# Kernel tuning notes

Measured on AMD Instinct MI355X. Metric: run time of the kernel, lower is better.

The kernel has to match this reference:

```python
import jax, jax.numpy as jnp
import numpy as np

EMBED_DIM = 1024
NUM_HEADS = 16
HEAD_DIM = EMBED_DIM // NUM_HEADS


def setup_inputs() -> dict:
    key = jax.random.key(0)
    k1, k2, k3 = jax.random.split(key, 3)
    scale = 1.0 / np.sqrt(EMBED_DIM)
    x = jax.random.normal(k1, (2, 2048, EMBED_DIM), dtype=jnp.float32)
    w_qkv = jax.random.normal(k2, (EMBED_DIM, 3 * EMBED_DIM), dtype=jnp.float32) * scale
    b_qkv = jnp.zeros((3 * EMBED_DIM,), dtype=jnp.float32)
    w_out = jax.random.normal(k3, (EMBED_DIM, EMBED_DIM), dtype=jnp.float32) * scale
    b_out = jnp.zeros((EMBED_DIM,), dtype=jnp.float32)
    return {"x": x, "w_qkv": w_qkv, "b_qkv": b_qkv, "w_out": w_out, "b_out": b_out}


def reference(x, w_qkv, b_qkv, w_out, b_out):
    B, N, C = x.shape
    H, D = NUM_HEADS, HEAD_DIM
    qkv = x @ w_qkv + b_qkv                      # [B, N, 3C]
    qkv = qkv.reshape(B, N, 3, H, D)
    q = qkv[:, :, 0].transpose(0, 2, 1, 3)       # [B, H, N, D]
    k = qkv[:, :, 1].transpose(0, 2, 1, 3)
    v = qkv[:, :, 2].transpose(0, 2, 1, 3)
    scores = jnp.einsum('bhnd,bhmd->bhnm', q, k) / jnp.sqrt(jnp.float32(D))
    attn = jax.nn.softmax(scores, axis=-1)
    out = jnp.einsum('bhnm,bhmd->bhnd', attn, v)  # [B, H, N, D]
    out = out.transpose(0, 2, 1, 3).reshape(B, N, C)
    return out @ w_out + b_out
```

## Files before the change

### kernel.cpp

```cpp
#include <hip/hip_runtime.h>
#include <stdint.h>

typedef unsigned short u16;
typedef short s16x8 __attribute__((ext_vector_type(8)));
typedef unsigned short u16x8 __attribute__((ext_vector_type(8)));
typedef unsigned short u16x4 __attribute__((ext_vector_type(4)));
typedef float f32x4 __attribute__((ext_vector_type(4)));
typedef float f32x16 __attribute__((ext_vector_type(16)));
typedef unsigned int u32x2 __attribute__((ext_vector_type(2)));
typedef unsigned int u32x4 __attribute__((ext_vector_type(4)));

#if __has_builtin(__builtin_amdgcn_exp2f)
#define EXP2F(x) __builtin_amdgcn_exp2f(x)
#else
#define EXP2F(x) exp2f(x)
#endif

#define QSCALE 0.18033688011112042f

__device__ __forceinline__ u16 f2b(float f) {
  union { float f; uint32_t u; } v; v.f = f;
  uint32_t r = (v.u + 0x7fffu + ((v.u >> 16) & 1u)) >> 16;
  return (u16)r;
}

__device__ __forceinline__ uint32_t pkhi(uint32_t hi, uint32_t lo) {
#if __has_builtin(__builtin_amdgcn_perm)
  return __builtin_amdgcn_perm(hi, lo, 0x07060302u);
#else
  return (lo >> 16) | (hi & 0xffff0000u);
#endif
}

__device__ __forceinline__ void plswap(uint32_t& a, uint32_t& b) {
#if __has_builtin(__builtin_amdgcn_permlane32_swap)
  typedef unsigned int uv2 __attribute__((ext_vector_type(2)));
  uv2 r = __builtin_amdgcn_permlane32_swap(a, b, false, false);
  a = r[0];
  b = r[1];
#else
  asm volatile("v_permlane32_swap_b32 %0, %1" : "+v"(a), "+v"(b));
#endif
}

__device__ __forceinline__ void sync_lds() {
  asm volatile("s_waitcnt lgkmcnt(0)\ns_barrier" ::: "memory");
}

__device__ __forceinline__ void gld16(const void* g, void* l) {
  __builtin_amdgcn_global_load_lds((__attribute__((address_space(1))) void*)g,
                                   (__attribute__((address_space(3))) void*)l,
                                   16, 0, 0);
}

__global__ __launch_bounds__(256)
void prep(const float* __restrict__ x, u16* __restrict__ xb,
          const float* __restrict__ w_qkv, u16* __restrict__ wqT,
          const float* __restrict__ w_out, u16* __restrict__ woT) {
  __shared__ float tile[32][33];
  const int bid = blockIdx.x;
  const int t = threadIdx.x;
  if (bid < 2048) {
    const size_t i = ((size_t)bid * 256 + t) * 8;
    f32x4 v0 = *(const f32x4*)(x + i);
    f32x4 v1 = *(const f32x4*)(x + i + 4);
    u16x8 u;
#pragma unroll
    for (int j = 0; j < 4; j++) { u[j] = f2b(v0[j]); u[4 + j] = f2b(v1[j]); }
    *(u16x8*)(xb + i) = u;
    return;
  }
  const float* src;
  u16* dst;
  int N, nb, kb;
  if (bid < 5120) {
    const int b2 = bid - 2048;
    src = w_qkv; dst = wqT; N = 3072;
    nb = (b2 % 96) * 32; kb = (b2 / 96) * 32;
  } else {
    const int b3 = bid - 5120;
    src = w_out; dst = woT; N = 1024;
    nb = (b3 & 31) * 32; kb = (b3 >> 5) * 32;
  }
  const int tx = t & 31, ty = t >> 5;
#pragma unroll
  for (int i = 0; i < 4; i++)
    tile[ty + i * 8][tx] = src[(size_t)(kb + ty + i * 8) * N + nb + tx];
  __syncthreads();
#pragma unroll
  for (int i = 0; i < 4; i++)
    dst[(size_t)(nb + ty + i * 8) * 1024 + kb + tx] = f2b(tile[tx][ty + i * 8]);
}

template <int EPI, int WN>
__global__ __launch_bounds__(256, 3)
void gemm_bt(const u16* __restrict__ A, const u16* __restrict__ Bt,
             const float* __restrict__ bias, float* __restrict__ outF,
             u16* __restrict__ outQ, u16* __restrict__ outK,
             u16* __restrict__ outVt, int M, int N, int K) {
  constexpr int BN = WN * 64;
  constexpr int RW = 4 / WN;
  constexpr int MI = 128 / RW / 16;
  constexpr int NBI = WN * 2;
  constexpr int SMEM = (EPI == 0) ? 34816 : (16384 + WN * 8192);
  __shared__ char smem[SMEM];
  u16* As = (u16*)smem;
  u16* Bs = As + 128 * 64;

  const int t = threadIdx.x;
  const int m0 = blockIdx.y * 128, n0 = blockIdx.x * BN;
  const int w = t >> 6, lane = t & 63;
  const int wm = w / WN, wn = w % WN;
  const int quad = lane >> 4, lrow = lane & 15;
  const int r8 = lane >> 3, s8 = lane & 7;
  const int csw = (s8 ^ r8) * 8;

  const u16* gA = A + (size_t)(m0 + w * 32 + r8) * K + csw;
  const u16* gB = Bt + (size_t)(n0 + w * (WN * 16) + r8) * K + csw;
  u16* wAs = As + (w * 32 + r8) * 64 + s8 * 8;
  u16* wBs = Bs + (w * (WN * 16) + r8) * 64 + s8 * 8;

  f32x4 acc[MI][4];
#pragma unroll
  for (int i = 0; i < MI; i++)
#pragma unroll
    for (int j = 0; j < 4; j++) {
      f32x4 z = {0.f, 0.f, 0.f, 0.f};
      acc[i][j] = z;
    }

  u16x8 pa[4], pb[NBI];
#pragma unroll
  for (int i = 0; i < 4; i++) pa[i] = *(const u16x8*)(gA + (size_t)(i * 8) * K);
#pragma unroll
  for (int i = 0; i < NBI; i++) pb[i] = *(const u16x8*)(gB + (size_t)(i * 8) * K);

  const int KT = K >> 6;
  for (int kt = 0; kt < KT; ++kt) {
    sync_lds();
#pragma unroll
    for (int i = 0; i < 4; i++) *(u16x8*)(wAs + i * 8 * 64) = pa[i];
#pragma unroll
    for (int i = 0; i < NBI; i++) *(u16x8*)(wBs + i * 8 * 64) = pb[i];
    if (kt + 1 < KT) {
      const size_t off = (size_t)(kt + 1) * 64;
#pragma unroll
      for (int i = 0; i < 4; i++)
        pa[i] = *(const u16x8*)(gA + (size_t)(i * 8) * K + off);
#pragma unroll
      for (int i = 0; i < NBI; i++)
        pb[i] = *(const u16x8*)(gB + (size_t)(i * 8) * K + off);
    }
    sync_lds();

#pragma unroll
    for (int ks = 0; ks < 2; ks++) {
      s16x8 a[MI], b[4];
#pragma unroll
      for (int i = 0; i < MI; i++)
        a[i] = *(const s16x8*)&As[(wm * (MI * 16) + i * 16 + lrow) * 64 +
                                  (((ks * 4 + quad) ^ (lrow & 7)) * 8)];
#pragma unroll
      for (int j = 0; j < 4; j++)
        b[j] = *(const s16x8*)&Bs[(wn * 64 + j * 16 + lrow) * 64 +
                                  (((ks * 4 + quad) ^ (lrow & 7)) * 8)];
#pragma unroll
      for (int i = 0; i < MI; i++)
#pragma unroll
        for (int j = 0; j < 4; j++)
          acc[i][j] = __builtin_amdgcn_mfma_f32_16x16x32_bf16(a[i], b[j],
                                                              acc[i][j], 0, 0, 0);
    }
  }

  if (EPI == 1) {
#pragma unroll
    for (int i = 0; i < MI; i++) {
      const int row = m0 + wm * (MI * 16) + i * 16 + quad * 4;
#pragma unroll
      for (int j = 0; j < 4; j++) {
        const int col = n0 + wn * 64 + j * 16 + lrow;
        const float bv = bias[col];
#pragma unroll
        for (int r = 0; r < 4; r++)
          outF[(size_t)(row + r) * N + col] = acc[i][j][r] + bv;
      }
    }
    return;
  }

  sync_lds();
  u16* rp = (u16*)smem + w * (64 * 68);
  const int cb = n0 + wn * 64;
  const int which = cb >> 10;
  const int h = (cb & 1023) >> 6;
  const int rbase = m0 + wm * 64;
  const int bb = rbase >> 11, nn0 = rbase & 2047;
  const int rl = lane >> 3, cc = (lane & 7) * 8;

  if (which != 2) {
    const float s = (which == 0) ? QSCALE : 1.0f;
#pragma unroll
    for (int i = 0; i < 4; i++)
#pragma unroll
      for (int j = 0; j < 4; j++) {
        const float bv = bias[cb + j * 16 + lrow];
#pragma unroll
        for (int r = 0; r < 4; r++)
          rp[(i * 16 + quad * 4 + r) * 68 + j * 16 + lrow] =
              f2b((acc[i][j][r] + bv) * s);
      }
    u16* dst = ((which == 0) ? outQ : outK) +
               ((size_t)(bb * 16 + h) * 2048 + nn0) * 64;
#pragma unroll
    for (int it = 0; it < 8; it++) {
      const int row = it * 8 + rl;
      *(u16x8*)&dst[(size_t)row * 64 + cc] = *(const u16x8*)&rp[row * 68 + cc];
    }
  } else {
#pragma unroll
    for (int i = 0; i < 4; i++)
#pragma unroll
      for (int j = 0; j < 4; j++) {
        const float bv = bias[cb + j * 16 + lrow];
        u16x4 pk;
#pragma unroll
        for (int r = 0; r < 4; r++) pk[r] = f2b(acc[i][j][r] + bv);
        *(u16x4*)&rp[(j * 16 + lrow) * 68 + i * 16 + quad * 4] = pk;
      }
    u16* dst = outVt + ((size_t)(bb * 16 + h) * 64) * 2048 + nn0;
#pragma unroll
    for (int it = 0; it < 8; it++) {
      const int d = it * 8 + rl;
      *(u16x8*)&dst[(size_t)d * 2048 + cc] = *(const u16x8*)&rp[d * 68 + cc];
    }
  }
}

__global__ __launch_bounds__(256)
void attn_kernel(const u16* __restrict__ Q, const u16* __restrict__ Kg,
                 const u16* __restrict__ Vt, u16* __restrict__ AO) {
  __shared__ u16 Ks[2][64 * 64];
  __shared__ u16 Vs[2][64 * 64];

  const int t = threadIdx.x;
  const int bh = blockIdx.x;
  const int qt = blockIdx.y;
  const int w = t >> 6, lane = t & 63;
  const int l31 = lane & 31, lh = lane >> 5;
  const int srow8 = lane >> 3, chunk = lane & 7;
  const int csw = chunk ^ srow8;
  const size_t base = (size_t)bh * 2048 * 64;

  s16x8 qf[4];
  {
    const u16* qp = Q + base + (size_t)(qt * 128 + w * 32 + l31) * 64 + lh * 8;
#pragma unroll
    for (int ks = 0; ks < 4; ks++) qf[ks] = *(const s16x8*)(qp + ks * 16);
  }

  int cx[4];
#pragma unroll
  for (int ks = 0; ks < 4; ks++) cx[ks] = ((2 * ks + lh) ^ (l31 & 7)) * 8;

  const u16* kgl = Kg + base + (size_t)(w * 16 + srow8) * 64 + csw * 8;
  const u16* vgl = Vt + base + (size_t)(w * 16 + srow8) * 2048 + csw * 8;
  const int lbase = (w * 16) * 64;

  const short one_bf16 = 0x3F80;
  s16x8 ones = {one_bf16, one_bf16, one_bf16, one_bf16,
                one_bf16, one_bf16, one_bf16, one_bf16};

  f32x16 ot0, ot1, liacc;
#pragma unroll
  for (int e = 0; e < 16; e++) { ot0[e] = 0.f; ot1[e] = 0.f; liacc[e] = 0.f; }

  gld16(kgl, &Ks[0][lbase]);
  gld16(kgl + 512, &Ks[0][lbase + 512]);
  gld16(vgl, &Vs[0][lbase]);
  gld16(vgl + (size_t)8 * 2048, &Vs[0][lbase + 512]);

  for (int kt = 0; kt < 32; kt++) {
    const int cur = kt & 1;
    __syncthreads();
    if (kt + 1 < 32) {
      const int nxt = cur ^ 1;
      gld16(kgl + (size_t)(kt + 1) * 4096, &Ks[nxt][lbase]);
      gld16(kgl + (size_t)(kt + 1) * 4096 + 512, &Ks[nxt][lbase + 512]);
      gld16(vgl + (kt + 1) * 64, &Vs[nxt][lbase]);
      gld16(vgl + (kt + 1) * 64 + (size_t)8 * 2048, &Vs[nxt][lbase + 512]);
    }

    f32x16 sc0, sc1;
#pragma unroll
    for (int e = 0; e < 16; e++) { sc0[e] = 0.f; sc1[e] = 0.f; }
#pragma unroll
    for (int ks = 0; ks < 4; ks++) {
      s16x8 k0 = *(const s16x8*)&Ks[cur][l31 * 64 + cx[ks]];
      s16x8 k1 = *(const s16x8*)&Ks[cur][(32 + l31) * 64 + cx[ks]];
      sc0 = __builtin_amdgcn_mfma_f32_32x32x16_bf16(k0, qf[ks], sc0, 0, 0, 0);
      sc1 = __builtin_amdgcn_mfma_f32_32x32x16_bf16(k1, qf[ks], sc1, 0, 0, 0);
    }

    uint32_t P[2][4][2];
#pragma unroll
    for (int tb = 0; tb < 2; tb++) {
      const f32x16& s = tb ? sc1 : sc0;
#pragma unroll
      for (int g = 0; g < 4; g++) {
        uint32_t u[4];
#pragma unroll
        for (int r = 0; r < 4; r++)
          u[r] = __builtin_bit_cast(uint32_t, EXP2F(s[g * 4 + r]));
        P[tb][g][0] = pkhi(u[1], u[0]);
        P[tb][g][1] = pkhi(u[3], u[2]);
      }
    }

#pragma unroll
    for (int tb = 0; tb < 2; tb++) {
#pragma unroll
      for (int gp = 0; gp < 2; gp++) {
        uint32_t w0 = P[tb][2 * gp][0], w2 = P[tb][2 * gp + 1][0];
        uint32_t w1 = P[tb][2 * gp][1], w3 = P[tb][2 * gp + 1][1];
        plswap(w0, w2);
        plswap(w1, w3);
        u32x4 fw = {w0, w1, w2, w3};
        s16x8 pf = __builtin_bit_cast(s16x8, fw);
        const int ks = tb * 2 + gp;
        s16x8 v0 = *(const s16x8*)&Vs[cur][l31 * 64 + cx[ks]];
        s16x8 v1 = *(const s16x8*)&Vs[cur][(32 + l31) * 64 + cx[ks]];
        ot0 = __builtin_amdgcn_mfma_f32_32x32x16_bf16(v0, pf, ot0, 0, 0, 0);
        ot1 = __builtin_amdgcn_mfma_f32_32x32x16_bf16(v1, pf, ot1, 0, 0, 0);
        liacc = __builtin_amdgcn_mfma_f32_32x32x16_bf16(ones, pf, liacc, 0, 0, 0);
      }
    }
  }

  const float inv = 1.0f / liacc[0];
  const int bb = bh >> 4, h = bh & 15;
  const int qn = qt * 128 + w * 32 + l31;
  u16* dst = AO + (size_t)(bb * 2048 + qn) * 1024 + h * 64;
#pragma unroll
  for (int db = 0; db < 2; db++) {
    const f32x16& o = db ? ot1 : ot0;
#pragma unroll
    for (int g = 0; g < 4; g++) {
      u16x4 pk;
#pragma unroll
      for (int r = 0; r < 4; r++) pk[r] = f2b(o[g * 4 + r] * inv);
      *(u16x4*)&dst[db * 32 + g * 8 + lh * 4] = pk;
    }
  }
}

extern "C" void kernel_launch(void* const* d_in, const int* in_sizes, int n_in,
                              void* d_out, int out_size, void* d_ws,
                              size_t ws_size, hipStream_t stream) {
  const float* x     = (const float*)d_in[0];
  const float* w_qkv = (const float*)d_in[1];
  const float* b_qkv = (const float*)d_in[2];
  const float* w_out = (const float*)d_in[3];
  const float* b_out = (const float*)d_in[4];
  float* out = (float*)d_out;

  char* ws = (char*)d_ws;
  u16* wqT = (u16*)ws; ws += (size_t)3072 * 1024 * 2;
  u16* woT = (u16*)ws; ws += (size_t)1024 * 1024 * 2;
  u16* q   = (u16*)ws; ws += (size_t)32 * 2048 * 64 * 2;
  u16* k   = (u16*)ws; ws += (size_t)32 * 2048 * 64 * 2;
  u16* vt  = (u16*)ws; ws += (size_t)32 * 64 * 2048 * 2;
  u16* xb  = (u16*)ws; ws += (size_t)4096 * 1024 * 2;
  u16* ao  = xb;

  prep<<<dim3(6144), 256, 0, stream>>>(x, xb, w_qkv, wqT, w_out, woT);
  gemm_bt<0, 2><<<dim3(24, 32), 256, 0, stream>>>(xb, wqT, b_qkv, nullptr, q, k,
                                                  vt, 4096, 3072, 1024);
  attn_kernel<<<dim3(32, 16), 256, 0, stream>>>(q, k, vt, ao);
  gemm_bt<1, 1><<<dim3(16, 32), 256, 0, stream>>>(ao, woT, b_out, out, nullptr,
                                                  nullptr, nullptr, 4096, 1024, 1024);
}
```

Measured before the change: 182.7 us.

## Split attention keys across two waves with register-direct K/V loads

Rewrites the attention kernel so each 128-thread block handles 64 queries. The two waves each process half of the key sequence, loading K and V fragments straight from global memory into registers, where the old kernel used double-buffered LDS staging with block barriers. The row sum is now accumulated in scalar registers rather than through an extra MFMA against a ones vector. Partial outputs are merged through shared memory at the end. This removes per-tile barriers and LDS traffic, at the cost of uncoalesced global loads with no LDS reuse, doubled K/V reads across query tiles, and a final reduction.

After: 192.0 us. 1.05x slower.

```diff
diff --git a/kernel.cpp b/kernel.cpp
--- a/kernel.cpp
+++ b/kernel.cpp
@@ -45,12 +45,6 @@
 
 __device__ __forceinline__ void sync_lds() {
   asm volatile("s_waitcnt lgkmcnt(0)\ns_barrier" ::: "memory");
-}
-
-__device__ __forceinline__ void gld16(const void* g, void* l) {
-  __builtin_amdgcn_global_load_lds((__attribute__((address_space(1))) void*)g,
-                                   (__attribute__((address_space(3))) void*)l,
-                                   16, 0, 0);
 }
 
 __global__ __launch_bounds__(256)
@@ -237,119 +231,150 @@
   }
 }
 
-__global__ __launch_bounds__(256)
+__global__ __launch_bounds__(128, 2)
 void attn_kernel(const u16* __restrict__ Q, const u16* __restrict__ Kg,
                  const u16* __restrict__ Vt, u16* __restrict__ AO) {
-  __shared__ u16 Ks[2][64 * 64];
-  __shared__ u16 Vs[2][64 * 64];
+  __shared__ float Osh[64][64];
+  __shared__ float Lsh[2][32];
 
   const int t = threadIdx.x;
   const int bh = blockIdx.x;
   const int qt = blockIdx.y;
   const int w = t >> 6, lane = t & 63;
   const int l31 = lane & 31, lh = lane >> 5;
-  const int srow8 = lane >> 3, chunk = lane & 7;
-  const int csw = chunk ^ srow8;
   const size_t base = (size_t)bh * 2048 * 64;
 
-  s16x8 qf[4];
-  {
-    const u16* qp = Q + base + (size_t)(qt * 128 + w * 32 + l31) * 64 + lh * 8;
-#pragma unroll
-    for (int ks = 0; ks < 4; ks++) qf[ks] = *(const s16x8*)(qp + ks * 16);
-  }
-
-  int cx[4];
-#pragma unroll
-  for (int ks = 0; ks < 4; ks++) cx[ks] = ((2 * ks + lh) ^ (l31 & 7)) * 8;
-
-  const u16* kgl = Kg + base + (size_t)(w * 16 + srow8) * 64 + csw * 8;
-  const u16* vgl = Vt + base + (size_t)(w * 16 + srow8) * 2048 + csw * 8;
-  const int lbase = (w * 16) * 64;
-
-  const short one_bf16 = 0x3F80;
-  s16x8 ones = {one_bf16, one_bf16, one_bf16, one_bf16,
-                one_bf16, one_bf16, one_bf16, one_bf16};
-
-  f32x16 ot0, ot1, liacc;
-#pragma unroll
-  for (int e = 0; e < 16; e++) { ot0[e] = 0.f; ot1[e] = 0.f; liacc[e] = 0.f; }
-
-  gld16(kgl, &Ks[0][lbase]);
-  gld16(kgl + 512, &Ks[0][lbase + 512]);
-  gld16(vgl, &Vs[0][lbase]);
-  gld16(vgl + (size_t)8 * 2048, &Vs[0][lbase + 512]);
+  s16x8 qf[2][4];
+#pragma unroll
+  for (int qg = 0; qg < 2; qg++) {
+    const u16* qp =
+        Q + base + (size_t)(qt * 64 + qg * 32 + l31) * 64 + lh * 8;
+#pragma unroll
+    for (int ks = 0; ks < 4; ks++) qf[qg][ks] = *(const s16x8*)(qp + ks * 16);
+  }
+
+  const u16* kp = Kg + base + (size_t)(w * 1024 + l31) * 64 + lh * 8;
+  const u16* vp = Vt + base + (size_t)l31 * 2048 + w * 1024 + lh * 8;
+
+  f32x16 ot[2][2];
+#pragma unroll
+  for (int qg = 0; qg < 2; qg++)
+#pragma unroll
+    for (int dt = 0; dt < 2; dt++)
+#pragma unroll
+      for (int e = 0; e < 16; e++) ot[qg][dt][e] = 0.f;
+  float li[2] = {0.f, 0.f};
+
+  s16x8 kf[4], vf[2][2];
+#pragma unroll
+  for (int ks = 0; ks < 4; ks++) kf[ks] = *(const s16x8*)(kp + ks * 16);
+#pragma unroll
+  for (int dt = 0; dt < 2; dt++)
+#pragma unroll
+    for (int s = 0; s < 2; s++)
+      vf[dt][s] = *(const s16x8*)(vp + (size_t)dt * 32 * 2048 + s * 16);
 
   for (int kt = 0; kt < 32; kt++) {
-    const int cur = kt & 1;
-    __syncthreads();
+    f32x16 sc[2];
+#pragma unroll
+    for (int qg = 0; qg < 2; qg++)
+#pragma unroll
+      for (int e = 0; e < 16; e++) sc[qg][e] = 0.f;
+#pragma unroll
+    for (int ks = 0; ks < 4; ks++) {
+      sc[0] = __builtin_amdgcn_mfma_f32_32x32x16_bf16(kf[ks], qf[0][ks], sc[0], 0, 0, 0);
+      sc[1] = __builtin_amdgcn_mfma_f32_32x32x16_bf16(kf[ks], qf[1][ks], sc[1], 0, 0, 0);
+    }
     if (kt + 1 < 32) {
-      const int nxt = cur ^ 1;
-      gld16(kgl + (size_t)(kt + 1) * 4096, &Ks[nxt][lbase]);
-      gld16(kgl + (size_t)(kt + 1) * 4096 + 512, &Ks[nxt][lbase + 512]);
-      gld16(vgl + (kt + 1) * 64, &Vs[nxt][lbase]);
-      gld16(vgl + (kt + 1) * 64 + (size_t)8 * 2048, &Vs[nxt][lbase + 512]);
-    }
-
-    f32x16 sc0, sc1;
-#pragma unroll
-    for (int e = 0; e < 16; e++) { sc0[e] = 0.f; sc1[e] = 0.f; }
-#pragma unroll
-    for (int ks = 0; ks < 4; ks++) {
-      s16x8 k0 = *(const s16x8*)&Ks[cur][l31 * 64 + cx[ks]];
-      s16x8 k1 = *(const s16x8*)&Ks[cur][(32 + l31) * 64 + cx[ks]];
-      sc0 = __builtin_amdgcn_mfma_f32_32x32x16_bf16(k0, qf[ks], sc0, 0, 0, 0);
-      sc1 = __builtin_amdgcn_mfma_f32_32x32x16_bf16(k1, qf[ks], sc1, 0, 0, 0);
+      const u16* kn = kp + (size_t)(kt + 1) * 2048;
+#pragma unroll
+      for (int ks = 0; ks < 4; ks++) kf[ks] = *(const s16x8*)(kn + ks * 16);
     }
 
     uint32_t P[2][4][2];
 #pragma unroll
-    for (int tb = 0; tb < 2; tb++) {
-      const f32x16& s = tb ? sc1 : sc0;
+    for (int qg = 0; qg < 2; qg++) {
+      float rsum = 0.f;
 #pragma unroll
       for (int g = 0; g < 4; g++) {
         uint32_t u[4];
 #pragma unroll
-        for (int r = 0; r < 4; r++)
-          u[r] = __builtin_bit_cast(uint32_t, EXP2F(s[g * 4 + r]));
-        P[tb][g][0] = pkhi(u[1], u[0]);
-        P[tb][g][1] = pkhi(u[3], u[2]);
-      }
-    }
-
-#pragma unroll
-    for (int tb = 0; tb < 2; tb++) {
-#pragma unroll
-      for (int gp = 0; gp < 2; gp++) {
-        uint32_t w0 = P[tb][2 * gp][0], w2 = P[tb][2 * gp + 1][0];
-        uint32_t w1 = P[tb][2 * gp][1], w3 = P[tb][2 * gp + 1][1];
+        for (int r = 0; r < 4; r++) {
+          u[r] = __builtin_bit_cast(uint32_t, EXP2F(sc[qg][g * 4 + r]));
+          rsum += __builtin_bit_cast(float, u[r] & 0xffff0000u);
+        }
+        P[qg][g][0] = pkhi(u[1], u[0]);
+        P[qg][g][1] = pkhi(u[3], u[2]);
+      }
+      li[qg] += rsum;
+    }
+
+#pragma unroll
+    for (int gp = 0; gp < 2; gp++) {
+      s16x8 pf[2];
+#pragma unroll
+      for (int qg = 0; qg < 2; qg++) {
+        uint32_t w0 = P[qg][2 * gp][0], w2 = P[qg][2 * gp + 1][0];
+        uint32_t w1 = P[qg][2 * gp][1], w3 = P[qg][2 * gp + 1][1];
         plswap(w0, w2);
         plswap(w1, w3);
         u32x4 fw = {w0, w1, w2, w3};
-        s16x8 pf = __builtin_bit_cast(s16x8, fw);
-        const int ks = tb * 2 + gp;
-        s16x8 v0 = *(const s16x8*)&Vs[cur][l31 * 64 + cx[ks]];
-        s16x8 v1 = *(const s16x8*)&Vs[cur][(32 + l31) * 64 + cx[ks]];
-        ot0 = __builtin_amdgcn_mfma_f32_32x32x16_bf16(v0, pf, ot0, 0, 0, 0);
-        ot1 = __builtin_amdgcn_mfma_f32_32x32x16_bf16(v1, pf, ot1, 0, 0, 0);
-        liacc = __builtin_amdgcn_mfma_f32_32x32x16_bf16(ones, pf, liacc, 0, 0, 0);
-      }
-    }
-  }
-
-  const float inv = 1.0f / liacc[0];
-  const int bb = bh >> 4, h = bh & 15;
-  const int qn = qt * 128 + w * 32 + l31;
-  u16* dst = AO + (size_t)(bb * 2048 + qn) * 1024 + h * 64;
-#pragma unroll
-  for (int db = 0; db < 2; db++) {
-    const f32x16& o = db ? ot1 : ot0;
-#pragma unroll
-    for (int g = 0; g < 4; g++) {
-      u16x4 pk;
-#pragma unroll
-      for (int r = 0; r < 4; r++) pk[r] = f2b(o[g * 4 + r] * inv);
-      *(u16x4*)&dst[db * 32 + g * 8 + lh * 4] = pk;
+        pf[qg] = __builtin_bit_cast(s16x8, fw);
+      }
+#pragma unroll
+      for (int dt = 0; dt < 2; dt++) {
+        ot[0][dt] = __builtin_amdgcn_mfma_f32_32x32x16_bf16(vf[dt][gp], pf[0], ot[0][dt], 0, 0, 0);
+        ot[1][dt] = __builtin_amdgcn_mfma_f32_32x32x16_bf16(vf[dt][gp], pf[1], ot[1][dt], 0, 0, 0);
+      }
+    }
+    if (kt + 1 < 32) {
+      const u16* vn = vp + (kt + 1) * 32;
+#pragma unroll
+      for (int dt = 0; dt < 2; dt++)
+#pragma unroll
+        for (int s = 0; s < 2; s++)
+          vf[dt][s] = *(const s16x8*)(vn + (size_t)dt * 32 * 2048 + s * 16);
+    }
+  }
+
+  float lifull[2];
+#pragma unroll
+  for (int qg = 0; qg < 2; qg++)
+    lifull[qg] = li[qg] + __shfl_xor(li[qg], 32);
+
+  if (w == 1) {
+#pragma unroll
+    for (int qg = 0; qg < 2; qg++) {
+#pragma unroll
+      for (int dt = 0; dt < 2; dt++)
+#pragma unroll
+        for (int e = 0; e < 16; e++)
+          Osh[qg * 32 + dt * 16 + e][lane] = ot[qg][dt][e];
+      if (lh == 0) Lsh[qg][l31] = lifull[qg];
+    }
+  }
+  __syncthreads();
+  if (w == 0) {
+    const int bb = bh >> 4, h = bh & 15;
+#pragma unroll
+    for (int qg = 0; qg < 2; qg++) {
+      const float inv = 1.0f / (lifull[qg] + Lsh[qg][l31]);
+      const int qn = qt * 64 + qg * 32 + l31;
+      u16* dst = AO + (size_t)(bb * 2048 + qn) * 1024 + h * 64;
+#pragma unroll
+      for (int dt = 0; dt < 2; dt++) {
+#pragma unroll
+        for (int g = 0; g < 4; g++) {
+          u16x4 pk;
+#pragma unroll
+          for (int r = 0; r < 4; r++) {
+            const float v =
+                ot[qg][dt][g * 4 + r] + Osh[qg * 32 + dt * 16 + g * 4 + r][lane];
+            pk[r] = f2b(v * inv);
+          }
+          *(u16x4*)&dst[dt * 32 + g * 8 + lh * 4] = pk;
+        }
+      }
     }
   }
 }
@@ -376,7 +401,7 @@
   prep<<<dim3(6144), 256, 0, stream>>>(x, xb, w_qkv, wqT, w_out, woT);
   gemm_bt<0, 2><<<dim3(24, 32), 256, 0, stream>>>(xb, wqT, b_qkv, nullptr, q, k,
                                                   vt, 4096, 3072, 1024);
-  attn_kernel<<<dim3(32, 16), 256, 0, stream>>>(q, k, vt, ao);
+  attn_kernel<<<dim3(32, 32), 128, 0, stream>>>(q, k, vt, ao);
   gemm_bt<1, 1><<<dim3(16, 32), 256, 0, stream>>>(ao, woT, b_out, out, nullptr,
                                                   nullptr, nullptr, 4096, 1024, 1024);
 }
```

## Split attention KV sequence across two wave groups per block and merge

Applied to the files above, without the earlier changes.

Doubles the attention block to 512 threads, with two groups of four waves each processing half of the key/value sequence (split-K) in their own shared-memory double buffers. At the end, the second group writes its partial output and row sums to shared memory and the first group combines them, normalizes and stores. The aim is to halve the serial KV loop per wave and raise the number of waves in flight per block, without needing more blocks. The cost is double the shared memory per block and an extra reduction through LDS. Since no running max is used, the partials add directly.

Result: faster. 173.1 us (-5.3%).

```diff
diff --git a/kernel.cpp b/kernel.cpp
--- a/kernel.cpp
+++ b/kernel.cpp
@@ -237,16 +237,18 @@
   }
 }
 
-__global__ __launch_bounds__(256)
+__global__ __launch_bounds__(512, 4)
 void attn_kernel(const u16* __restrict__ Q, const u16* __restrict__ Kg,
                  const u16* __restrict__ Vt, u16* __restrict__ AO) {
-  __shared__ u16 Ks[2][64 * 64];
-  __shared__ u16 Vs[2][64 * 64];
+  __shared__ u16 Ks[2][2][64 * 64];
+  __shared__ u16 Vs[2][2][64 * 64];
+  __shared__ float Lsh[4][32];
 
   const int t = threadIdx.x;
   const int bh = blockIdx.x;
   const int qt = blockIdx.y;
   const int w = t >> 6, lane = t & 63;
+  const int kh = w >> 2, wi = w & 3;
   const int l31 = lane & 31, lh = lane >> 5;
   const int srow8 = lane >> 3, chunk = lane & 7;
   const int csw = chunk ^ srow8;
@@ -254,7 +256,7 @@
 
   s16x8 qf[4];
   {
-    const u16* qp = Q + base + (size_t)(qt * 128 + w * 32 + l31) * 64 + lh * 8;
+    const u16* qp = Q + base + (size_t)(qt * 128 + wi * 32 + l31) * 64 + lh * 8;
 #pragma unroll
     for (int ks = 0; ks < 4; ks++) qf[ks] = *(const s16x8*)(qp + ks * 16);
   }
@@ -263,9 +265,11 @@
 #pragma unroll
   for (int ks = 0; ks < 4; ks++) cx[ks] = ((2 * ks + lh) ^ (l31 & 7)) * 8;
 
-  const u16* kgl = Kg + base + (size_t)(w * 16 + srow8) * 64 + csw * 8;
-  const u16* vgl = Vt + base + (size_t)(w * 16 + srow8) * 2048 + csw * 8;
-  const int lbase = (w * 16) * 64;
+  const u16* kgl = Kg + base + (size_t)(kh * 1024 + wi * 16 + srow8) * 64 +
+                   csw * 8;
+  const u16* vgl = Vt + base + (size_t)(wi * 16 + srow8) * 2048 + kh * 1024 +
+                   csw * 8;
+  const int lbase = (wi * 16) * 64;
 
   const short one_bf16 = 0x3F80;
   s16x8 ones = {one_bf16, one_bf16, one_bf16, one_bf16,
@@ -275,20 +279,20 @@
 #pragma unroll
   for (int e = 0; e < 16; e++) { ot0[e] = 0.f; ot1[e] = 0.f; liacc[e] = 0.f; }
 
-  gld16(kgl, &Ks[0][lbase]);
-  gld16(kgl + 512, &Ks[0][lbase + 512]);
-  gld16(vgl, &Vs[0][lbase]);
-  gld16(vgl + (size_t)8 * 2048, &Vs[0][lbase + 512]);
-
-  for (int kt = 0; kt < 32; kt++) {
+  gld16(kgl, &Ks[kh][0][lbase]);
+  gld16(kgl + 512, &Ks[kh][0][lbase + 512]);
+  gld16(vgl, &Vs[kh][0][lbase]);
+  gld16(vgl + (size_t)8 * 2048, &Vs[kh][0][lbase + 512]);
+
+  for (int kt = 0; kt < 16; kt++) {
     const int cur = kt & 1;
     __syncthreads();
-    if (kt + 1 < 32) {
+    if (kt + 1 < 16) {
       const int nxt = cur ^ 1;
-      gld16(kgl + (size_t)(kt + 1) * 4096, &Ks[nxt][lbase]);
-      gld16(kgl + (size_t)(kt + 1) * 4096 + 512, &Ks[nxt][lbase + 512]);
-      gld16(vgl + (kt + 1) * 64, &Vs[nxt][lbase]);
-      gld16(vgl + (kt + 1) * 64 + (size_t)8 * 2048, &Vs[nxt][lbase + 512]);
+      gld16(kgl + (size_t)(kt + 1) * 4096, &Ks[kh][nxt][lbase]);
+      gld16(kgl + (size_t)(kt + 1) * 4096 + 512, &Ks[kh][nxt][lbase + 512]);
+      gld16(vgl + (kt + 1) * 64, &Vs[kh][nxt][lbase]);
+      gld16(vgl + (kt + 1) * 64 + (size_t)8 * 2048, &Vs[kh][nxt][lbase + 512]);
     }
 
     f32x16 sc0, sc1;
@@ -296,8 +300,8 @@
     for (int e = 0; e < 16; e++) { sc0[e] = 0.f; sc1[e] = 0.f; }
 #pragma unroll
     for (int ks = 0; ks < 4; ks++) {
-      s16x8 k0 = *(const s16x8*)&Ks[cur][l31 * 64 + cx[ks]];
-      s16x8 k1 = *(const s16x8*)&Ks[cur][(32 + l31) * 64 + cx[ks]];
+      s16x8 k0 = *(const s16x8*)&Ks[kh][cur][l31 * 64 + cx[ks]];
+      s16x8 k1 = *(const s16x8*)&Ks[kh][cur][(32 + l31) * 64 + cx[ks]];
       sc0 = __builtin_amdgcn_mfma_f32_32x32x16_bf16(k0, qf[ks], sc0, 0, 0, 0);
       sc1 = __builtin_amdgcn_mfma_f32_32x32x16_bf16(k1, qf[ks], sc1, 0, 0, 0);
     }
@@ -328,8 +332,8 @@
         u32x4 fw = {w0, w1, w2, w3};
         s16x8 pf = __builtin_bit_cast(s16x8, fw);
         const int ks = tb * 2 + gp;
-        s16x8 v0 = *(const s16x8*)&Vs[cur][l31 * 64 + cx[ks]];
-        s16x8 v1 = *(const s16x8*)&Vs[cur][(32 + l31) * 64 + cx[ks]];
+        s16x8 v0 = *(const s16x8*)&Vs[kh][cur][l31 * 64 + cx[ks]];
+        s16x8 v1 = *(const s16x8*)&Vs[kh][cur][(32 + l31) * 64 + cx[ks]];
         ot0 = __builtin_amdgcn_mfma_f32_32x32x16_bf16(v0, pf, ot0, 0, 0, 0);
         ot1 = __builtin_amdgcn_mfma_f32_32x32x16_bf16(v1, pf, ot1, 0, 0, 0);
         liacc = __builtin_amdgcn_mfma_f32_32x32x16_bf16(ones, pf, liacc, 0, 0, 0);
@@ -337,19 +341,37 @@
     }
   }
 
-  const float inv = 1.0f / liacc[0];
-  const int bb = bh >> 4, h = bh & 15;
-  const int qn = qt * 128 + w * 32 + l31;
-  u16* dst = AO + (size_t)(bb * 2048 + qn) * 1024 + h * 64;
-#pragma unroll
-  for (int db = 0; db < 2; db++) {
-    const f32x16& o = db ? ot1 : ot0;
-#pragma unroll
-    for (int g = 0; g < 4; g++) {
-      u16x4 pk;
-#pragma unroll
-      for (int r = 0; r < 4; r++) pk[r] = f2b(o[g * 4 + r] * inv);
-      *(u16x4*)&dst[db * 32 + g * 8 + lh * 4] = pk;
+  float* Osm = (float*)Ks;
+  const float lihalf = liacc[0];
+  __syncthreads();
+  if (kh == 1) {
+#pragma unroll
+    for (int e = 0; e < 16; e++) {
+      Osm[((wi * 2 + 0) * 16 + e) * 64 + lane] = ot0[e];
+      Osm[((wi * 2 + 1) * 16 + e) * 64 + lane] = ot1[e];
+    }
+    if (lh == 0) Lsh[wi][l31] = lihalf;
+  }
+  __syncthreads();
+  if (kh == 0) {
+    const float inv = 1.0f / (lihalf + Lsh[wi][l31]);
+    const int bb = bh >> 4, h = bh & 15;
+    const int qn = qt * 128 + wi * 32 + l31;
+    u16* dst = AO + (size_t)(bb * 2048 + qn) * 1024 + h * 64;
+#pragma unroll
+    for (int dt = 0; dt < 2; dt++) {
+      const f32x16& o = dt ? ot1 : ot0;
+#pragma unroll
+      for (int g = 0; g < 4; g++) {
+        u16x4 pk;
+#pragma unroll
+        for (int r = 0; r < 4; r++) {
+          const float v =
+              o[g * 4 + r] + Osm[((wi * 2 + dt) * 16 + g * 4 + r) * 64 + lane];
+          pk[r] = f2b(v * inv);
+        }
+        *(u16x4*)&dst[dt * 32 + g * 8 + lh * 4] = pk;
+      }
     }
   }
 }
@@ -376,7 +398,7 @@
   prep<<<dim3(6144), 256, 0, stream>>>(x, xb, w_qkv, wqT, w_out, woT);
   gemm_bt<0, 2><<<dim3(24, 32), 256, 0, stream>>>(xb, wqT, b_qkv, nullptr, q, k,
                                                   vt, 4096, 3072, 1024);
-  attn_kernel<<<dim3(32, 16), 256, 0, stream>>>(q, k, vt, ao);
+  attn_kernel<<<dim3(32, 16), 512, 0, stream>>>(q, k, vt, ao);
   gemm_bt<1, 1><<<dim3(16, 32), 256, 0, stream>>>(ao, woT, b_out, out, nullptr,
                                                   nullptr, nullptr, 4096, 1024, 1024);
 }
```
